# Performance work log

Hardware: AMD Instinct MI355X
Metric: run time of the kernel (lower is better)

## Reference

```python
import jax, jax.numpy as jnp
import numpy as np

VOCAB, EMB, HID = 50257, 256, 512
B, S = 64, 512


def setup_inputs() -> dict:
    key = jax.random.key(0)
    ks = jax.random.split(key, 11)
    sc = 0.05
    return {
        "inputs": jax.random.randint(ks[0], (B, S), 0, VOCAB, dtype=jnp.int32),
        "emb": jax.random.normal(ks[1], (VOCAB, EMB), jnp.float32) * sc,
        "Wi": jax.random.normal(ks[2], (EMB, 4 * HID), jnp.float32) * sc,   # kernel, gate order i|f|g|o (Keras)
        "Wh": jax.random.normal(ks[3], (HID, 4 * HID), jnp.float32) * sc,   # recurrent kernel
        "b": jax.random.normal(ks[4], (4 * HID,), jnp.float32) * sc,
        "W1": jax.random.normal(ks[5], (HID, HID), jnp.float32) * sc,
        "b1": jnp.zeros((HID,), jnp.float32),
        "W2": jax.random.normal(ks[6], (HID, HID), jnp.float32) * sc,
        "b2": jnp.zeros((HID,), jnp.float32),
        "W3": jax.random.normal(ks[7], (HID, VOCAB), jnp.float32) * sc,
        "b3": jnp.zeros((VOCAB,), jnp.float32),
    }


def _lstm_final_h(x, Wi, Wh, b):
    # x: [B, S, E] -> final hidden state [B, H]
    Bsz = x.shape[0]
    H = Wh.shape[0]
    h0 = jnp.zeros((Bsz, H), x.dtype)
    c0 = jnp.zeros((Bsz, H), x.dtype)

    def step(carry, xt):
        h, c = carry
        z = xt @ Wi + h @ Wh + b              # [B, 4H]
        i, f, g, o = jnp.split(z, 4, axis=-1)  # Keras gate order: input, forget, cell, output
        i = jax.nn.sigmoid(i)
        f = jax.nn.sigmoid(f)
        g = jnp.tanh(g)
        o = jax.nn.sigmoid(o)
        c = f * c + i * g
        h = o * jnp.tanh(c)
        return (h, c), None

    (h, _), _ = jax.lax.scan(step, (h0, c0), jnp.swapaxes(x, 0, 1))  # scan over time [S, B, E]
    return h


def reference(inputs, emb, Wi, Wh, b, W1, b1, W2, b2, W3, b3):
    src_emb = emb[inputs]                      # [B, S, E] embedding lookup
    enc_hidden = _lstm_final_h(src_emb, Wi, Wh, b)  # [B, H]
    y = jnp.tanh(enc_hidden @ W1 + b1)
    y = jnp.tanh(y @ W2 + b2)
    logits = y @ W3 + b3                       # [B, vocab]
    return jax.nn.log_softmax(logits, axis=-1)
```

## Files before the change

kernel.cpp:

```cpp
#include <hip/hip_runtime.h>
#include <hip/hip_bf16.h>

#define VOCAB 50257
#define EMBD  256
#define HID   512
#define BATCH 64
#define SEQ   512

typedef short bf16x8 __attribute__((ext_vector_type(8)));
typedef float f32x4  __attribute__((ext_vector_type(4)));

__device__ inline short f2b(float f) {
    union { float f; unsigned u; } v; v.f = f;
    unsigned r = v.u + 0x7FFFu + ((v.u >> 16) & 1u);
    return (short)(r >> 16);
}
__device__ inline unsigned pack2_trunc(float lo, float hi) {
    union { float f; unsigned u; } a, b; a.f = lo; b.f = hi;
    return __builtin_amdgcn_perm(b.u, a.u, 0x07060302);
}
__device__ inline float fast_tanh(float x) {
    x = fminf(fmaxf(x, -15.f), 15.f);
    float e = __expf(2.f * x);
    return (e - 1.f) / (e + 1.f);
}
__device__ inline float fast_sig(float x) { return 1.f / (1.f + __expf(-x)); }

__device__ inline void load_x_frags(const float* __restrict__ emb, int idxv, int quad, bf16x8* Ax) {
#pragma unroll
    for (int kt = 0; kt < 8; ++kt) {
        const float* p = emb + (size_t)idxv * EMBD + kt * 32 + quad * 8;
        float4 e0 = *(const float4*)(p);
        float4 e1 = *(const float4*)(p + 4);
        union { bf16x8 v; unsigned u[4]; } f;
        f.u[0] = pack2_trunc(e0.x, e0.y);
        f.u[1] = pack2_trunc(e0.z, e0.w);
        f.u[2] = pack2_trunc(e1.x, e1.y);
        f.u[3] = pack2_trunc(e1.z, e1.w);
        Ax[kt] = f.v;
    }
}

__device__ inline void mirror_issue16(const unsigned long long* p, unsigned long long* v) {
    asm volatile(
        "global_load_dwordx2 %0,  %16, off sc0\n\t"
        "global_load_dwordx2 %1,  %16, off offset:512 sc0\n\t"
        "global_load_dwordx2 %2,  %16, off offset:1024 sc0\n\t"
        "global_load_dwordx2 %3,  %16, off offset:1536 sc0\n\t"
        "global_load_dwordx2 %4,  %17, off sc0\n\t"
        "global_load_dwordx2 %5,  %17, off offset:512 sc0\n\t"
        "global_load_dwordx2 %6,  %17, off offset:1024 sc0\n\t"
        "global_load_dwordx2 %7,  %17, off offset:1536 sc0\n\t"
        "global_load_dwordx2 %8,  %18, off sc0\n\t"
        "global_load_dwordx2 %9,  %18, off offset:512 sc0\n\t"
        "global_load_dwordx2 %10, %18, off offset:1024 sc0\n\t"
        "global_load_dwordx2 %11, %18, off offset:1536 sc0\n\t"
        "global_load_dwordx2 %12, %19, off sc0\n\t"
        "global_load_dwordx2 %13, %19, off offset:512 sc0\n\t"
        "global_load_dwordx2 %14, %19, off offset:1024 sc0\n\t"
        "global_load_dwordx2 %15, %19, off offset:1536 sc0"
        : "=&v"(v[0]), "=&v"(v[1]), "=&v"(v[2]), "=&v"(v[3]),
          "=&v"(v[4]), "=&v"(v[5]), "=&v"(v[6]), "=&v"(v[7]),
          "=&v"(v[8]), "=&v"(v[9]), "=&v"(v[10]), "=&v"(v[11]),
          "=&v"(v[12]), "=&v"(v[13]), "=&v"(v[14]), "=&v"(v[15])
        : "v"(p), "v"(p + 256), "v"(p + 512), "v"(p + 768)
        : "memory");
}
__device__ inline void vm_fence() {
    asm volatile("s_waitcnt vmcnt(0)" ::: "memory");
    __builtin_amdgcn_sched_barrier(0);
}

__global__ __launch_bounds__(256, 2) void lstm_kernel(
    const int* __restrict__ idx, const float* __restrict__ emb,
    const float* __restrict__ Wi, const float* __restrict__ Wh,
    const float* __restrict__ bvec,
    unsigned long long* __restrict__ hbuf ,
    unsigned long long* __restrict__ hmir ,
    unsigned short* __restrict__ hfinal )
{
    const int wgid = blockIdx.x;
    if ((wgid & 7) >= 4) return;
    const int grp  = wgid & 7;
    const int jj   = wgid >> 3;
    const int tid  = threadIdx.x;
    const int lane = tid & 63;
    const int w    = tid >> 6;
    const int quad = lane >> 4;
    const int l16  = lane & 15;
    const int cbase = jj * 16 + w * 4;
    const int wcol  = (l16 & 3) * HID + cbase + (l16 >> 2);
    const int arow  = grp * 16 + l16;

    __shared__ __align__(16) unsigned hstageF[2][4096];

    bf16x8 Bh[16], Bx[8];
#pragma unroll
    for (int kt = 0; kt < 16; ++kt)
#pragma unroll
        for (int i = 0; i < 8; ++i)
            Bh[kt][i] = f2b(Wh[(size_t)(kt * 32 + quad * 8 + i) * 2048 + wcol]);
#pragma unroll
    for (int kt = 0; kt < 8; ++kt)
#pragma unroll
        for (int i = 0; i < 8; ++i)
            Bx[kt][i] = f2b(Wi[(size_t)(kt * 32 + quad * 8 + i) * 2048 + wcol]);

    float bvr[4];
#pragma unroll
    for (int r = 0; r < 4; ++r) bvr[r] = bvec[r * HID + cbase + quad];

    bf16x8 Ax[8];
    load_x_frags(emb, idx[arow * SEQ], quad, Ax);

    const int scp = jj * 8 + w * 2 + (quad >> 1);
    const int su  = (scp >> 4) * 256 + ((scp >> 2) & 3) * 64 + l16 * 4 + (scp & 3);

    float cs = 0.f;
    bool mirSticky = true;

    for (int t = 0; t < SEQ; ++t) {
        const size_t off = (size_t)((t & 1) * 4 + grp) * 4096 + w * 1024 + lane;
        const unsigned long long* rbM = hbuf + off;
        const unsigned long long* rbL = hmir + off;
        bool useMir = mirSticky;

        unsigned long long v[16];
        if (t > 0) {
            if (useMir) {
                mirror_issue16(rbL, v);
            } else {
#pragma unroll
                for (int i = 0; i < 16; ++i)
                    v[i] = __hip_atomic_load(rbM + i * 64,
                                             __ATOMIC_RELAXED, __HIP_MEMORY_SCOPE_AGENT);
            }
        }

        f32x4 a0 = {0.f, 0.f, 0.f, 0.f}, a1 = {0.f, 0.f, 0.f, 0.f};
#pragma unroll
        for (int kt = 0; kt < 8; kt += 2) {
            a0 = __builtin_amdgcn_mfma_f32_16x16x32_bf16(Bx[kt],     Ax[kt],     a0, 0, 0, 0);
            a1 = __builtin_amdgcn_mfma_f32_16x16x32_bf16(Bx[kt + 1], Ax[kt + 1], a1, 0, 0, 0);
        }

        if (t > 0) {
            const unsigned tg = (unsigned)t;
            int rounds = 0;
            for (;;) {
                if (useMir) vm_fence();
                bool ok = true;
#pragma unroll
                for (int i = 0; i < 16; ++i)
                    ok = ok && ((unsigned)(v[i] >> 32) == tg);
                if (__ballot(ok) == ~0ull) break;
                if (useMir && ++rounds >= 32) useMir = false;
                if (useMir) {
                    mirror_issue16(rbL, v);
                } else {
#pragma unroll
                    for (int i = 0; i < 16; ++i)
                        v[i] = __hip_atomic_load(rbM + i * 64,
                                                 __ATOMIC_RELAXED, __HIP_MEMORY_SCOPE_AGENT);
                }
            }
            if (!useMir && t >= 8) mirSticky = false;
#pragma unroll
            for (int i = 0; i < 16; ++i)
                hstageF[t & 1][w * 1024 + i * 64 + lane] = (unsigned)v[i];
        }
        __syncthreads();

        if (t > 0) {
            const unsigned* hp = &hstageF[t & 1][0];
#pragma unroll
            for (int kt = 0; kt < 16; kt += 2) {
                bf16x8 ha = *(const bf16x8*)(hp + kt * 256 + lane * 4);
                bf16x8 hb = *(const bf16x8*)(hp + (kt + 1) * 256 + lane * 4);
                a0 = __builtin_amdgcn_mfma_f32_16x16x32_bf16(Bh[kt],     ha, a0, 0, 0, 0);
                a1 = __builtin_amdgcn_mfma_f32_16x16x32_bf16(Bh[kt + 1], hb, a1, 0, 0, 0);
            }
        }

        float iG = fast_sig (a0[0] + a1[0] + bvr[0]);
        float fG = fast_sig (a0[1] + a1[1] + bvr[1]);
        float gG = fast_tanh(a0[2] + a1[2] + bvr[2]);
        float oG = fast_sig (a0[3] + a1[3] + bvr[3]);
        cs = fG * cs + iG * gG;
        float h  = oG * fast_tanh(cs);
        float hp2 = __shfl_xor(h, 16);
        unsigned pv = (unsigned)(unsigned short)f2b(h) |
                      ((unsigned)(unsigned short)f2b(hp2) << 16);

        if ((quad & 1) == 0) {
            unsigned long long val = (unsigned long long)pv |
                                     ((unsigned long long)(unsigned)(t + 1) << 32);
            const size_t soff = (size_t)(((t + 1) & 1) * 4 + grp) * 4096 + su;
            __hip_atomic_store(hmir + soff, val, __ATOMIC_RELAXED,
                               __HIP_MEMORY_SCOPE_WORKGROUP);
            __hip_atomic_store(hbuf + soff, val, __ATOMIC_RELAXED,
                               __HIP_MEMORY_SCOPE_AGENT);
            if (t == SEQ - 1)
                *(unsigned*)&hfinal[(size_t)(grp * 16 + l16) * HID + cbase + quad] = pv;
        }

        if (t + 1 < SEQ) {
            int nx = idx[arow * SEQ + t + 1];
            load_x_frags(emb, nx, quad, Ax);
        }
    }
}

__global__ __launch_bounds__(256, 1) void gemm_tanh_kernel(
    const unsigned short* __restrict__ A, const float* __restrict__ W,
    const float* __restrict__ bias, unsigned short* __restrict__ out)
{
    const int tid = threadIdx.x, lane = tid & 63, wave = tid >> 6;
    const int quad = lane >> 4, l16 = lane & 15;
    const int col = blockIdx.x * 16 + l16;
    bf16x8 Bw[16];
#pragma unroll
    for (int kt = 0; kt < 16; ++kt)
#pragma unroll
        for (int i = 0; i < 8; ++i)
            Bw[kt][i] = f2b(W[(size_t)(kt * 32 + quad * 8 + i) * HID + col]);
    f32x4 acc = {0.f, 0.f, 0.f, 0.f};
#pragma unroll
    for (int kt = 0; kt < 16; ++kt) {
        bf16x8 a = *(const bf16x8*)(A + (size_t)(wave * 16 + l16) * HID + kt * 32 + quad * 8);
        acc = __builtin_amdgcn_mfma_f32_16x16x32_bf16(a, Bw[kt], acc, 0, 0, 0);
    }
    const float bvv = bias[col];
#pragma unroll
    for (int r = 0; r < 4; ++r) {
        float y = fast_tanh(acc[r] + bvv);
        out[(size_t)(wave * 16 + quad * 4 + r) * HID + col] = (unsigned short)f2b(y);
    }
}

__global__ __launch_bounds__(256, 2) void logits_kernel(
    const unsigned short* __restrict__ A, const float* __restrict__ W3,
    const float* __restrict__ b3, float* __restrict__ outL)
{
    const int tid = threadIdx.x, lane = tid & 63, wave = tid >> 6;
    const int quad = lane >> 4, l16 = lane & 15;
    const int c0 = blockIdx.x * 64;
    const int col = c0 + wave * 16 + l16;
    const bool cok = col < VOCAB;
    const int colc = cok ? col : (VOCAB - 1);

    __shared__ unsigned short wt[256][68];

    f32x4 acc[4];
#pragma unroll
    for (int rt = 0; rt < 4; ++rt) acc[rt] = (f32x4){0.f, 0.f, 0.f, 0.f};

    const int kr = tid >> 4;
    const int cg = (tid & 15) * 4;

    for (int kc = 0; kc < 2; ++kc) {
#pragma unroll 4
        for (int it = 0; it < 16; ++it) {
            const int k = it * 16 + kr;
            const int gc = c0 + cg;
            float4 wv;
            if (gc + 3 < VOCAB) {
                wv = *(const float4*)&W3[(size_t)(kc * 256 + k) * VOCAB + gc];
            } else {
                const float* Wr = &W3[(size_t)(kc * 256 + k) * VOCAB];
                wv.x = (gc + 0 < VOCAB) ? Wr[gc + 0] : 0.f;
                wv.y = (gc + 1 < VOCAB) ? Wr[gc + 1] : 0.f;
                wv.z = (gc + 2 < VOCAB) ? Wr[gc + 2] : 0.f;
                wv.w = (gc + 3 < VOCAB) ? Wr[gc + 3] : 0.f;
            }
            unsigned short* d = &wt[k][cg];
            d[0] = (unsigned short)f2b(wv.x);
            d[1] = (unsigned short)f2b(wv.y);
            d[2] = (unsigned short)f2b(wv.z);
            d[3] = (unsigned short)f2b(wv.w);
        }
        __syncthreads();
        bf16x8 Bw[8];
#pragma unroll
        for (int kt = 0; kt < 8; ++kt)
#pragma unroll
            for (int i = 0; i < 8; ++i)
                Bw[kt][i] = (short)wt[kt * 32 + quad * 8 + i][wave * 16 + l16];
#pragma unroll
        for (int rt = 0; rt < 4; ++rt)
#pragma unroll
            for (int kt = 0; kt < 8; ++kt) {
                bf16x8 a = *(const bf16x8*)(A + (size_t)(rt * 16 + l16) * HID +
                                            kc * 256 + kt * 32 + quad * 8);
                acc[rt] = __builtin_amdgcn_mfma_f32_16x16x32_bf16(a, Bw[kt], acc[rt], 0, 0, 0);
            }
        __syncthreads();
    }
    const float bvv = b3[colc];
    if (cok) {
#pragma unroll
        for (int rt = 0; rt < 4; ++rt)
#pragma unroll
            for (int r = 0; r < 4; ++r)
                outL[(size_t)(rt * 16 + quad * 4 + r) * VOCAB + col] = acc[rt][r] + bvv;
    }
}

__global__ __launch_bounds__(256, 1) void lsm_kernel(
    const float* __restrict__ lg, float* __restrict__ out)
{
    const int row = blockIdx.x;
    const float* L = lg + (size_t)row * VOCAB;
    const float4* L4 = (const float4*)L;
    const int nv4 = VOCAB / 4;

    float m = -1e30f;
    for (int i = threadIdx.x; i < nv4; i += 256) {
        float4 v = L4[i];
        m = fmaxf(fmaxf(fmaxf(m, v.x), fmaxf(v.y, v.z)), v.w);
    }
    if (threadIdx.x == 0) m = fmaxf(m, L[VOCAB - 1]);
#pragma unroll
    for (int o = 32; o; o >>= 1) m = fmaxf(m, __shfl_xor(m, o));
    __shared__ float red[4], red2[4];
    if ((threadIdx.x & 63) == 0) red[threadIdx.x >> 6] = m;
    __syncthreads();
    m = fmaxf(fmaxf(red[0], red[1]), fmaxf(red[2], red[3]));

    float s = 0.f;
    for (int i = threadIdx.x; i < nv4; i += 256) {
        float4 v = L4[i];
        s += __expf(v.x - m) + __expf(v.y - m) + __expf(v.z - m) + __expf(v.w - m);
    }
    if (threadIdx.x == 0) s += __expf(L[VOCAB - 1] - m);
#pragma unroll
    for (int o = 32; o; o >>= 1) s += __shfl_xor(s, o);
    if ((threadIdx.x & 63) == 0) red2[threadIdx.x >> 6] = s;
    __syncthreads();
    s = red2[0] + red2[1] + red2[2] + red2[3];
    const float ls = m + __logf(s);

    float* O = out + (size_t)row * VOCAB;
    float4* O4 = (float4*)O;
    for (int i = threadIdx.x; i < nv4; i += 256) {
        float4 v = L4[i];
        O4[i] = (float4){v.x - ls, v.y - ls, v.z - ls, v.w - ls};
    }
    if (threadIdx.x == 0) O[VOCAB - 1] = L[VOCAB - 1] - ls;
}

extern "C" void kernel_launch(void* const* d_in, const int* in_sizes, int n_in,
                              void* d_out, int out_size, void* d_ws, size_t ws_size,
                              hipStream_t stream) {
    (void)in_sizes; (void)n_in; (void)out_size; (void)ws_size;
    const int*   idx = (const int*)d_in[0];
    const float* emb = (const float*)d_in[1];
    const float* Wi  = (const float*)d_in[2];
    const float* Wh  = (const float*)d_in[3];
    const float* b   = (const float*)d_in[4];
    const float* W1  = (const float*)d_in[5];
    const float* b1  = (const float*)d_in[6];
    const float* W2  = (const float*)d_in[7];
    const float* b2  = (const float*)d_in[8];
    const float* W3  = (const float*)d_in[9];
    const float* b3  = (const float*)d_in[10];
    float* out = (float*)d_out;

    char* w = (char*)d_ws;
    unsigned long long* hbuf   = (unsigned long long*)w;
    unsigned short*     y1     = (unsigned short*)w;
    unsigned short*     y2     = (unsigned short*)(w + 65536);
    unsigned short*     hfinal = (unsigned short*)(w + 262144);
    unsigned long long* hmir   = (unsigned long long*)(w + 327680);
    float*              logits = (float*)(w + 262144);

    lstm_kernel<<<256, 256, 0, stream>>>(idx, emb, Wi, Wh, b, hbuf, hmir, hfinal);
    gemm_tanh_kernel<<<HID / 16, 256, 0, stream>>>(hfinal, W1, b1, y1);
    gemm_tanh_kernel<<<HID / 16, 256, 0, stream>>>(y1, W2, b2, y2);
    logits_kernel<<<(VOCAB + 63) / 64, 256, 0, stream>>>(y2, W3, b3, logits);
    lsm_kernel<<<BATCH, 256, 0, stream>>>(logits, out);
}
```

Before: 2.241 ms.

## Poll per-wave ready flags before fetching hidden-state data in LSTM recurrence

```diff
diff --git a/kernel.cpp b/kernel.cpp
--- a/kernel.cpp
+++ b/kernel.cpp
@@ -66,6 +66,12 @@
         : "v"(p), "v"(p + 256), "v"(p + 512), "v"(p + 768)
         : "memory");
 }
+__device__ inline void flag_issue2(const unsigned long long* p, unsigned long long* f) {
+    asm volatile(
+        "global_load_dwordx2 %0, %2, off sc0\n\t"
+        "global_load_dwordx2 %1, %2, off offset:512 sc0"
+        : "=&v"(f[0]), "=&v"(f[1]) : "v"(p) : "memory");
+}
 __device__ inline void vm_fence() {
     asm volatile("s_waitcnt vmcnt(0)" ::: "memory");
     __builtin_amdgcn_sched_barrier(0);
@@ -77,6 +83,8 @@
     const float* __restrict__ bvec,
     unsigned long long* __restrict__ hbuf ,
     unsigned long long* __restrict__ hmir ,
+    unsigned long long* __restrict__ flagM ,
+    unsigned long long* __restrict__ flagL ,
     unsigned short* __restrict__ hfinal )
 {
     const int wgid = blockIdx.x;
@@ -115,6 +123,7 @@
 
     const int scp = jj * 8 + w * 2 + (quad >> 1);
     const int su  = (scp >> 4) * 256 + ((scp >> 2) & 3) * 64 + l16 * 4 + (scp & 3);
+    const int pw  = jj * 4 + w;
 
     float cs = 0.f;
     bool mirSticky = true;
@@ -123,17 +132,17 @@
         const size_t off = (size_t)((t & 1) * 4 + grp) * 4096 + w * 1024 + lane;
         const unsigned long long* rbM = hbuf + off;
         const unsigned long long* rbL = hmir + off;
+        const unsigned long long* fbM = flagM + grp * 128 + lane;
+        const unsigned long long* fbL = flagL + grp * 128 + lane;
         bool useMir = mirSticky;
 
-        unsigned long long v[16];
+        unsigned long long f[2];
         if (t > 0) {
             if (useMir) {
-                mirror_issue16(rbL, v);
+                flag_issue2(fbL, f);
             } else {
-#pragma unroll
-                for (int i = 0; i < 16; ++i)
-                    v[i] = __hip_atomic_load(rbM + i * 64,
-                                             __ATOMIC_RELAXED, __HIP_MEMORY_SCOPE_AGENT);
+                f[0] = __hip_atomic_load(fbM,      __ATOMIC_RELAXED, __HIP_MEMORY_SCOPE_AGENT);
+                f[1] = __hip_atomic_load(fbM + 64, __ATOMIC_RELAXED, __HIP_MEMORY_SCOPE_AGENT);
             }
         }
 
@@ -144,25 +153,42 @@
             a1 = __builtin_amdgcn_mfma_f32_16x16x32_bf16(Bx[kt + 1], Ax[kt + 1], a1, 0, 0, 0);
         }
 
+        unsigned long long v[16];
         if (t > 0) {
             const unsigned tg = (unsigned)t;
-            int rounds = 0;
+            int frounds = 0;
             for (;;) {
                 if (useMir) vm_fence();
-                bool ok = true;
-#pragma unroll
-                for (int i = 0; i < 16; ++i)
-                    ok = ok && ((unsigned)(v[i] >> 32) == tg);
+                bool ok = ((unsigned)(f[0] >> 32) >= tg) &&
+                          ((unsigned)(f[1] >> 32) >= tg);
                 if (__ballot(ok) == ~0ull) break;
-                if (useMir && ++rounds >= 32) useMir = false;
+                __builtin_amdgcn_s_sleep(1);
+                if (useMir && ++frounds >= 64) useMir = false;
+                if (useMir) {
+                    flag_issue2(fbL, f);
+                } else {
+                    f[0] = __hip_atomic_load(fbM,      __ATOMIC_RELAXED, __HIP_MEMORY_SCOPE_AGENT);
+                    f[1] = __hip_atomic_load(fbM + 64, __ATOMIC_RELAXED, __HIP_MEMORY_SCOPE_AGENT);
+                }
+            }
+            int drounds = 0;
+            for (;;) {
                 if (useMir) {
                     mirror_issue16(rbL, v);
+                    vm_fence();
                 } else {
 #pragma unroll
                     for (int i = 0; i < 16; ++i)
                         v[i] = __hip_atomic_load(rbM + i * 64,
                                                  __ATOMIC_RELAXED, __HIP_MEMORY_SCOPE_AGENT);
                 }
+                bool ok = true;
+#pragma unroll
+                for (int i = 0; i < 16; ++i)
+                    ok = ok && ((unsigned)(v[i] >> 32) == tg);
+                if (__ballot(ok) == ~0ull) break;
+                if (useMir && ++drounds >= 16) useMir = false;
+                if (drounds >= 4) __builtin_amdgcn_s_sleep(1);
             }
             if (!useMir && t >= 8) mirSticky = false;
 #pragma unroll
@@ -202,6 +228,13 @@
                                __HIP_MEMORY_SCOPE_AGENT);
             if (t == SEQ - 1)
                 *(unsigned*)&hfinal[(size_t)(grp * 16 + l16) * HID + cbase + quad] = pv;
+        }
+        if (lane == 0) {
+            unsigned long long fv = ((unsigned long long)(unsigned)(t + 1) << 32) | 1u;
+            __hip_atomic_store(flagL + grp * 128 + pw, fv, __ATOMIC_RELAXED,
+                               __HIP_MEMORY_SCOPE_WORKGROUP);
+            __hip_atomic_store(flagM + grp * 128 + pw, fv, __ATOMIC_RELAXED,
+                               __HIP_MEMORY_SCOPE_AGENT);
         }
 
         if (t + 1 < SEQ) {
@@ -372,9 +405,11 @@
     unsigned short*     y2     = (unsigned short*)(w + 65536);
     unsigned short*     hfinal = (unsigned short*)(w + 262144);
     unsigned long long* hmir   = (unsigned long long*)(w + 327680);
+    unsigned long long* flagM  = (unsigned long long*)(w + 589824);
+    unsigned long long* flagL  = (unsigned long long*)(w + 593920);
     float*              logits = (float*)(w + 262144);
 
-    lstm_kernel<<<256, 256, 0, stream>>>(idx, emb, Wi, Wh, b, hbuf, hmir, hfinal);
+    lstm_kernel<<<256, 256, 0, stream>>>(idx, emb, Wi, Wh, b, hbuf, hmir, flagM, flagL, hfinal);
     gemm_tanh_kernel<<<HID / 16, 256, 0, stream>>>(hfinal, W1, b1, y1);
     gemm_tanh_kernel<<<HID / 16, 256, 0, stream>>>(y1, W2, b2, y2);
     logits_kernel<<<(VOCAB + 63) / 64, 256, 0, stream>>>(y2, W3, b3, logits);
```

Measured after the change: 2.394 ms. 6.8% more time.
